# Optimization experiments

Hardware: AMD Instinct MI355X
Metric: run time of the kernel (lower is better)

The kernel has to match this reference:

```python
import jax, jax.numpy as jnp
import numpy as np
from jax import lax

V, Dm, NL, N, K, E = 32000, 1024, 4, 16, 4, 2
Di = Dm * E
B, T = 1, 2048
EPS = 1e-5


def setup_inputs() -> dict:
    key = jax.random.key(0)
    ks = jax.random.split(key, 8)
    s = 0.02
    A_init = jnp.log(jnp.arange(1.0, N + 1, dtype=jnp.float32))  # (N,)
    return {
        "idx": jax.random.randint(ks[0], (B, T), 0, V),
        "emb": jax.random.normal(ks[1], (V, Dm), dtype=jnp.float32) * s,
        "norm_w": jnp.ones((NL, Dm), jnp.float32),
        "in_proj_w": jax.random.normal(ks[2], (NL, 2 * Di, Dm), dtype=jnp.float32) * s,
        "conv_w": jax.random.normal(ks[3], (NL, Di, 1, K), dtype=jnp.float32) * s,
        "conv_b": jnp.zeros((NL, Di), jnp.float32),
        "x_proj_w": jax.random.normal(ks[4], (NL, 2 * N + 1, Di), dtype=jnp.float32) * s,
        "dt_proj_w": jax.random.normal(ks[5], (NL, Di, 1), dtype=jnp.float32) * s,
        "dt_proj_b": jnp.zeros((NL, Di), jnp.float32),
        "A_log": jnp.broadcast_to(A_init[None, None, :], (NL, Di, N)).copy(),
        "D_param": jnp.ones((NL, Di), jnp.float32),
        "out_proj_w": jax.random.normal(ks[6], (NL, Dm, Di), dtype=jnp.float32) * s,
        "norm_f_w": jnp.ones((Dm,), jnp.float32),
    }


def _rmsnorm(x, w):
    rms = jnp.sqrt(jnp.mean(x * x, axis=-1, keepdims=True) + EPS)
    return x / rms * w


def _mamba_block(x, in_w, cw, cb, xp_w, dt_w, dt_b, A_log, Dp, out_w):
    # x: (B, L, Dm)
    xz = x @ in_w.T                       # (B, L, 2*Di)
    x_ssm, z = xz[..., :Di], xz[..., Di:]
    # causal depthwise conv (torch pads both sides then crops -> left-pad only)
    xc = x_ssm.transpose(0, 2, 1)         # (B, Di, L)
    xc = lax.conv_general_dilated(
        xc, cw, window_strides=(1,), padding=[(K - 1, 0)],
        dimension_numbers=("NCH", "OIH", "NCH"), feature_group_count=Di)
    xc = xc + cb[None, :, None]
    u = jax.nn.silu(xc.transpose(0, 2, 1))  # (B, L, Di)
    # selective SSM
    A = -jnp.exp(A_log)                     # (Di, N)
    xp = u @ xp_w.T                         # (B, L, 2N+1)
    dt_raw, Bv, Cv = xp[..., :1], xp[..., 1:1 + N], xp[..., 1 + N:]
    dt = jax.nn.softplus(dt_raw * dt_w[:, 0] + dt_b)  # (B, L, Di)

    def step(h, inp):
        dt_t, Bv_t, Cv_t, u_t = inp          # (B,Di),(B,N),(B,N),(B,Di)
        dA = jnp.exp(dt_t[..., None] * A)    # (B, Di, N)
        h = dA * h + (dt_t * u_t)[..., None] * Bv_t[:, None, :]
        y_t = jnp.einsum("bdn,bn->bd", h, Cv_t)
        return h, y_t

    h0 = jnp.zeros((x.shape[0], Di, N), u.dtype)
    xs = (dt.transpose(1, 0, 2), Bv.transpose(1, 0, 2),
          Cv.transpose(1, 0, 2), u.transpose(1, 0, 2))
    _, ys = lax.scan(step, h0, xs)           # (L, B, Di)
    y = ys.transpose(1, 0, 2) + u * Dp
    y = y * jax.nn.silu(z)
    return y @ out_w.T


def reference(idx, emb, norm_w, in_proj_w, conv_w, conv_b, x_proj_w,
              dt_proj_w, dt_proj_b, A_log, D_param, out_proj_w, norm_f_w):
    x = emb[idx]                             # (B, T, Dm); dropout=0 in eval
    for l in range(NL):
        x = x + _mamba_block(_rmsnorm(x, norm_w[l]), in_proj_w[l], conv_w[l],
                             conv_b[l], x_proj_w[l], dt_proj_w[l], dt_proj_b[l],
                             A_log[l], D_param[l], out_proj_w[l])
    x = _rmsnorm(x, norm_f_w)
    logits = x @ emb.T                       # tied lm_head
    return logits
```

## Files before the change

### kernel.cpp

```cpp
#include <hip/hip_runtime.h>
#include <hip/hip_bf16.h>

typedef __hip_bfloat16 bf16;
typedef __attribute__((ext_vector_type(8))) short short8;
typedef __attribute__((ext_vector_type(4))) float f32x4;

#define TT 2048
#define DM 1024
#define DI 2048
#define NLAYER 4
#define NST 16
#define KC 4
#define VOCAB 32000
#define XPS 33
#define NCHUNK 64
#define CLEN 32

__device__ __forceinline__ float us2f(unsigned short u) {
    union { float f; unsigned int i; } c; c.i = ((unsigned int)u) << 16; return c.f;
}
__device__ __forceinline__ float ldin(const void* p, size_t i, int f32) {
    return f32 ? ((const float*)p)[i] : us2f(((const unsigned short*)p)[i]);
}
__device__ __forceinline__ unsigned short f2us(float f) {
    bf16 h = __float2bfloat16(f);
    return *(unsigned short*)&h;
}

__global__ void detect_kernel(const unsigned int* __restrict__ w_bits, int* __restrict__ flag) {
    if (threadIdx.x == 0) *flag = (w_bits[0] == 0x3F800000u) ? 1 : 0;
}

__global__ void cvt8_kernel(const float* __restrict__ s, unsigned short* __restrict__ d, int n8) {
    int i = blockIdx.x * 256 + threadIdx.x;
    if (i >= n8) return;
    float4 a = ((const float4*)s)[2 * i];
    float4 b = ((const float4*)s)[2 * i + 1];
    unsigned int w0 = (unsigned int)f2us(a.x) | ((unsigned int)f2us(a.y) << 16);
    unsigned int w1 = (unsigned int)f2us(a.z) | ((unsigned int)f2us(a.w) << 16);
    unsigned int w2 = (unsigned int)f2us(b.x) | ((unsigned int)f2us(b.y) << 16);
    unsigned int w3 = (unsigned int)f2us(b.z) | ((unsigned int)f2us(b.w) << 16);
    ((uint4*)d)[i] = make_uint4(w0, w1, w2, w3);
}

__global__ void embed_kernel(const int* __restrict__ idx, const void* __restrict__ emb,
                             float* __restrict__ x, const int* __restrict__ fl) {
    int f32 = *fl;
    int i = blockIdx.x * 256 + threadIdx.x;
    int t = i >> 10, d = i & 1023;
    x[i] = ldin(emb, (size_t)idx[t] * DM + d, f32);
}

__global__ void rmsnorm_kernel(const float* __restrict__ x, const void* __restrict__ w,
                               size_t wofs, bf16* __restrict__ ob, const int* __restrict__ fl) {
    int f32 = *fl;
    int t = blockIdx.x, tid = threadIdx.x;
    float s = 0.f;
    for (int i = tid; i < DM; i += 256) { float v = x[(size_t)t * DM + i]; s += v * v; }
    __shared__ float red[256];
    red[tid] = s; __syncthreads();
    for (int st = 128; st > 0; st >>= 1) { if (tid < st) red[tid] += red[tid + st]; __syncthreads(); }
    float inv = rsqrtf(red[0] / (float)DM + 1e-5f);
    for (int i = tid; i < DM; i += 256) {
        float v = x[(size_t)t * DM + i] * inv * ldin(w, wofs + i, f32);
        ob[(size_t)t * DM + i] = __float2bfloat16(v);
    }
}

__global__ __launch_bounds__(256, 2)
void gemm_mfma(const bf16* __restrict__ A16, const bf16* __restrict__ B16,
               const float* __restrict__ Res, float* __restrict__ Cf, bf16* __restrict__ C16,
               int MT, int NT, int Kk) {
    int Nn = NT << 7;
    __shared__ __align__(16) unsigned short As[128 * 32];
    __shared__ __align__(16) unsigned short Bs[128 * 32];
    int tid = threadIdx.x;
    int w = tid >> 6, lane = tid & 63;
    int h = lane >> 4, r = lane & 15;

    int nwg = MT * NT;
    int bid = blockIdx.x;
    int swz = ((nwg & 7) == 0) ? ((bid & 7) * (nwg >> 3) + (bid >> 3)) : bid;
    int mt = swz % MT, nt = swz / MT;
    int m0 = mt << 7, n0 = nt << 7;

    const unsigned short* Ap = (const unsigned short*)A16;
    const unsigned short* Bp = (const unsigned short*)B16;

    int srow = (w << 5) + (lane >> 2);
    int skof = (lane & 3) << 3;
    const unsigned short* gA = Ap + (size_t)(m0 + srow) * Kk + skof;
    const unsigned short* gB = Bp + (size_t)(n0 + srow) * Kk + skof;
    unsigned short* lA = As + (w << 10);
    unsigned short* lB = Bs + (w << 10);

    f32x4 acc[4][4];
#pragma unroll
    for (int i = 0; i < 4; i++)
#pragma unroll
        for (int j = 0; j < 4; j++) acc[i][j] = (f32x4){0.f, 0.f, 0.f, 0.f};

    int wr = w >> 1, wc = w & 1;
    const unsigned short* rA = As + (((wr << 6) + r) << 5) + (h << 3);
    const unsigned short* rB = Bs + (((wc << 6) + r) << 5) + (h << 3);

    for (int k0 = 0; k0 < Kk; k0 += 32) {
        __builtin_amdgcn_global_load_lds(
            (const __attribute__((address_space(1))) void*)(gA + k0),
            (__attribute__((address_space(3))) void*)lA, 16, 0, 0);
        __builtin_amdgcn_global_load_lds(
            (const __attribute__((address_space(1))) void*)(gA + k0 + (size_t)16 * Kk),
            (__attribute__((address_space(3))) void*)(lA + 512), 16, 0, 0);
        __builtin_amdgcn_global_load_lds(
            (const __attribute__((address_space(1))) void*)(gB + k0),
            (__attribute__((address_space(3))) void*)lB, 16, 0, 0);
        __builtin_amdgcn_global_load_lds(
            (const __attribute__((address_space(1))) void*)(gB + k0 + (size_t)16 * Kk),
            (__attribute__((address_space(3))) void*)(lB + 512), 16, 0, 0);
        __syncthreads();
        short8 af[4], bfr[4];
#pragma unroll
        for (int mi = 0; mi < 4; mi++) af[mi] = *(const short8*)(rA + (mi << 9));
#pragma unroll
        for (int ni = 0; ni < 4; ni++) bfr[ni] = *(const short8*)(rB + (ni << 9));
#pragma unroll
        for (int mi = 0; mi < 4; mi++)
#pragma unroll
            for (int ni = 0; ni < 4; ni++)
                acc[mi][ni] = __builtin_amdgcn_mfma_f32_16x16x32_bf16(
                    af[mi], bfr[ni], acc[mi][ni], 0, 0, 0);
        __syncthreads();
    }
#pragma unroll
    for (int mi = 0; mi < 4; mi++) {
#pragma unroll
        for (int j = 0; j < 4; j++) {
            int row = m0 + (wr << 6) + (mi << 4) + (h << 2) + j;
            size_t base = (size_t)row * Nn + n0 + (wc << 6) + r;
#pragma unroll
            for (int ni = 0; ni < 4; ni++) {
                float v = acc[mi][ni][j];
                size_t o = base + (ni << 4);
                if (Res) v += Res[o];
                if (Cf)  Cf[o] = v;
                if (C16) C16[o] = __float2bfloat16(v);
            }
        }
    }
}

__global__ void convsilu_kernel(const float* __restrict__ xz, const void* __restrict__ cw,
                                size_t cwofs, const void* __restrict__ cb, size_t cbofs,
                                float* __restrict__ u, const int* __restrict__ fl) {
    int f32 = *fl;
    int i = blockIdx.x * 256 + threadIdx.x;
    int t = i >> 11, d = i & 2047;
    float s = ldin(cb, cbofs + d, f32);
#pragma unroll
    for (int j = 0; j < KC; j++) {
        int tt = t - (KC - 1) + j;
        if (tt >= 0) s += ldin(cw, cwofs + d * KC + j, f32) * xz[(size_t)tt * (2 * DI) + d];
    }
    u[i] = s / (1.f + __expf(-s));
}

__global__ void xproj_kernel(const float* __restrict__ u, const void* __restrict__ xpw,
                             size_t wofs, float* __restrict__ xp, const int* __restrict__ fl) {
    int f32 = *fl;
    int t = blockIdx.x, tid = threadIdx.x;
    int w = tid >> 6, lane = tid & 63;
    const float* up = u + (size_t)t * DI + tid * 8;
    float4 u0 = *(const float4*)up;
    float4 u1 = *(const float4*)(up + 4);
    float a0 = u0.x, a1 = u0.y, a2 = u0.z, a3 = u0.w;
    float a4 = u1.x, a5 = u1.y, a6 = u1.z, a7 = u1.w;
    float p[XPS];
    if (f32) {
        const float* wb = (const float*)xpw + wofs + tid * 8;
#pragma unroll
        for (int n = 0; n < XPS; n++) {
            const float* wp = wb + (size_t)n * DI;
            float4 w0 = *(const float4*)wp, w1 = *(const float4*)(wp + 4);
            p[n] = a0 * w0.x + a1 * w0.y + a2 * w0.z + a3 * w0.w
                 + a4 * w1.x + a5 * w1.y + a6 * w1.z + a7 * w1.w;
        }
    } else {
        const unsigned short* wb = (const unsigned short*)xpw + wofs + tid * 8;
#pragma unroll
        for (int n = 0; n < XPS; n++) {
            uint4 wv = *(const uint4*)(wb + (size_t)n * DI);
            p[n] = a0 * us2f(wv.x & 0xffff) + a1 * us2f(wv.x >> 16)
                 + a2 * us2f(wv.y & 0xffff) + a3 * us2f(wv.y >> 16)
                 + a4 * us2f(wv.z & 0xffff) + a5 * us2f(wv.z >> 16)
                 + a6 * us2f(wv.w & 0xffff) + a7 * us2f(wv.w >> 16);
        }
    }
    __shared__ float red[4 * XPS];
#pragma unroll
    for (int n = 0; n < XPS; n++) {
        float v = p[n];
#pragma unroll
        for (int s_ = 1; s_ < 64; s_ <<= 1) v += __shfl_xor(v, s_, 64);
        if (lane == 0) red[w * XPS + n] = v;
    }
    __syncthreads();
    if (tid < XPS)
        xp[t * XPS + tid] = red[tid] + red[XPS + tid] + red[2 * XPS + tid] + red[3 * XPS + tid];
}

__global__ void scanA_kernel(const float* __restrict__ xp, const float* __restrict__ u,
                             const void* __restrict__ dtw, size_t dtwofs,
                             const void* __restrict__ dtb, size_t dtbofs,
                             const void* __restrict__ A_log, size_t aofs,
                             float* __restrict__ S, float* __restrict__ hend,
                             const int* __restrict__ fl) {
    int f32 = *fl;
    int c = blockIdx.y;
    int d = blockIdx.x * 256 + threadIdx.x;
    __shared__ float xps[CLEN * XPS];
    for (int i = threadIdx.x; i < CLEN * XPS; i += 256) xps[i] = xp[c * CLEN * XPS + i];
    __syncthreads();
    float dw = ldin(dtw, dtwofs + d, f32);
    float db = ldin(dtb, dtbofs + d, f32);
    float Ar[NST], hh[NST];
#pragma unroll
    for (int n = 0; n < NST; n++) {
        Ar[n] = -expf(ldin(A_log, aofs + (size_t)d * NST + n, f32));
        hh[n] = 0.f;
    }
    float ssum = 0.f;
    const float* urow = u + (size_t)c * CLEN * DI + d;
    for (int tt = 0; tt < CLEN; tt++) {
        float s = xps[tt * XPS] * dw + db;
        float dtv = (s > 20.f) ? s : log1pf(__expf(s));
        float uv = urow[(size_t)tt * DI];
        float du = dtv * uv;
        ssum += dtv;
        const float* bb = &xps[tt * XPS + 1];
#pragma unroll
        for (int n = 0; n < NST; n++)
            hh[n] = __expf(dtv * Ar[n]) * hh[n] + du * bb[n];
    }
    S[c * DI + d] = ssum;
#pragma unroll
    for (int n = 0; n < NST; n++) hend[((size_t)c * DI + d) * NST + n] = hh[n];
}

__global__ void scanB_kernel(const float* __restrict__ S, float* __restrict__ hend,
                             const void* __restrict__ A_log, size_t aofs,
                             const int* __restrict__ fl) {
    int f32 = *fl;
    int i = blockIdx.x * 256 + threadIdx.x;
    int d = i >> 4;
    float A = -expf(ldin(A_log, aofs + i, f32));
    float H = 0.f;
    for (int c = 0; c < NCHUNK; c++) {
        size_t o = (size_t)c * (DI * NST) + i;
        float he = hend[o];
        hend[o] = H;
        H = __expf(A * S[c * DI + d]) * H + he;
    }
}

__global__ void scanC_kernel(const float* __restrict__ xp, const float* __restrict__ u,
                             const float* __restrict__ xz,
                             const void* __restrict__ dtw, size_t dtwofs,
                             const void* __restrict__ dtb, size_t dtbofs,
                             const void* __restrict__ A_log, size_t aofs,
                             const void* __restrict__ Dp, size_t dofs,
                             const float* __restrict__ hcar, bf16* __restrict__ y16,
                             const int* __restrict__ fl) {
    int f32 = *fl;
    int c = blockIdx.y;
    int d = blockIdx.x * 256 + threadIdx.x;
    __shared__ float xps[CLEN * XPS];
    for (int i = threadIdx.x; i < CLEN * XPS; i += 256) xps[i] = xp[c * CLEN * XPS + i];
    __syncthreads();
    float dw = ldin(dtw, dtwofs + d, f32);
    float db = ldin(dtb, dtbofs + d, f32);
    float Dpv = ldin(Dp, dofs + d, f32);
    float Ar[NST], hh[NST];
#pragma unroll
    for (int n = 0; n < NST; n++) {
        Ar[n] = -expf(ldin(A_log, aofs + (size_t)d * NST + n, f32));
        hh[n] = hcar[((size_t)c * DI + d) * NST + n];
    }
    for (int tt = 0; tt < CLEN; tt++) {
        int t = c * CLEN + tt;
        float s = xps[tt * XPS] * dw + db;
        float dtv = (s > 20.f) ? s : log1pf(__expf(s));
        float uv = u[(size_t)t * DI + d];
        float du = dtv * uv;
        const float* bb = &xps[tt * XPS + 1];
        const float* cc = &xps[tt * XPS + 1 + NST];
        float accv = 0.f;
#pragma unroll
        for (int n = 0; n < NST; n++) {
            hh[n] = __expf(dtv * Ar[n]) * hh[n] + du * bb[n];
            accv += hh[n] * cc[n];
        }
        float z = xz[(size_t)t * (2 * DI) + DI + d];
        float sz = z / (1.f + __expf(-z));
        y16[(size_t)t * DI + d] = __float2bfloat16((accv + uv * Dpv) * sz);
    }
}

extern "C" void kernel_launch(void* const* d_in, const int* in_sizes, int n_in,
                              void* d_out, int out_size, void* d_ws, size_t ws_size,
                              hipStream_t stream) {
    const int*  idx       = (const int*)d_in[0];
    const void* emb       = d_in[1];
    const void* norm_w    = d_in[2];
    const void* in_proj_w = d_in[3];
    const void* conv_w    = d_in[4];
    const void* conv_b    = d_in[5];
    const void* x_proj_w  = d_in[6];
    const void* dt_proj_w = d_in[7];
    const void* dt_proj_b = d_in[8];
    const void* A_log     = d_in[9];
    const void* D_param   = d_in[10];
    const void* out_proj_w= d_in[11];
    const void* norm_f_w  = d_in[12];

    float* ws   = (float*)d_ws;
    float* xz   = ws;
    float* u    = ws + 8388608;
    float* hend = ws + 12582912;
    bf16*  W16A = (bf16*)(ws + 14680064);
    bf16*  W16B = (bf16*)(ws + 16777216);
    float* S    = ws + 17825792;
    float* xp   = ws + 17956864;
    float* x    = ws + 18024448;
    bf16*  xn16 = (bf16*)(ws + 20121600);
    bf16*  y16  = (bf16*)(ws + 21170176);
    int*   fl   = (int*)(ws + 23267328);
    bf16*  emb16= (bf16*)ws;

    long long esz = in_sizes ? (long long)in_sizes[1] : -1;
    int isf32 = (esz == (long long)VOCAB * DM * 2) ? 0 : 1;

    detect_kernel<<<1, 64, 0, stream>>>((const unsigned int*)norm_w, fl);
    embed_kernel<<<TT * DM / 256, 256, 0, stream>>>(idx, emb, x, fl);

    for (int l = 0; l < NLAYER; l++) {
        const bf16* Bin;
        const bf16* Bout;
        if (isf32) {
            cvt8_kernel<<<2 * DI * DM / 8 / 256, 256, 0, stream>>>(
                (const float*)in_proj_w + (size_t)l * 2 * DI * DM,
                (unsigned short*)W16A, 2 * DI * DM / 8);
            cvt8_kernel<<<DM * DI / 8 / 256, 256, 0, stream>>>(
                (const float*)out_proj_w + (size_t)l * DM * DI,
                (unsigned short*)W16B, DM * DI / 8);
            Bin = W16A; Bout = W16B;
        } else {
            Bin  = (const bf16*)in_proj_w  + (size_t)l * 2 * DI * DM;
            Bout = (const bf16*)out_proj_w + (size_t)l * DM * DI;
        }

        rmsnorm_kernel<<<TT, 256, 0, stream>>>(x, norm_w, (size_t)l * DM, xn16, fl);
        gemm_mfma<<<(TT / 128) * (2 * DI / 128), 256, 0, stream>>>(
            xn16, Bin, nullptr, xz, nullptr, TT / 128, 2 * DI / 128, DM);
        convsilu_kernel<<<TT * DI / 256, 256, 0, stream>>>(
            xz, conv_w, (size_t)l * DI * KC, conv_b, (size_t)l * DI, u, fl);
        xproj_kernel<<<TT, 256, 0, stream>>>(u, x_proj_w, (size_t)l * XPS * DI, xp, fl);
        scanA_kernel<<<dim3(DI / 256, NCHUNK), 256, 0, stream>>>(
            xp, u, dt_proj_w, (size_t)l * DI, dt_proj_b, (size_t)l * DI,
            A_log, (size_t)l * DI * NST, S, hend, fl);
        scanB_kernel<<<DI * NST / 256, 256, 0, stream>>>(
            S, hend, A_log, (size_t)l * DI * NST, fl);
        scanC_kernel<<<dim3(DI / 256, NCHUNK), 256, 0, stream>>>(
            xp, u, xz, dt_proj_w, (size_t)l * DI, dt_proj_b, (size_t)l * DI,
            A_log, (size_t)l * DI * NST, D_param, (size_t)l * DI, hend, y16, fl);
        gemm_mfma<<<(TT / 128) * (DM / 128), 256, 0, stream>>>(
            y16, Bout, x, x, nullptr, TT / 128, DM / 128, DI);
    }

    rmsnorm_kernel<<<TT, 256, 0, stream>>>(x, norm_f_w, 0, xn16, fl);

    const bf16* Bemb;
    if (isf32) {
        cvt8_kernel<<<VOCAB * DM / 8 / 256, 256, 0, stream>>>(
            (const float*)emb, (unsigned short*)emb16, VOCAB * DM / 8);
        Bemb = emb16;
    } else {
        Bemb = (const bf16*)emb;
    }
    if (isf32)
        gemm_mfma<<<(TT / 128) * (VOCAB / 128), 256, 0, stream>>>(
            xn16, Bemb, nullptr, (float*)d_out, nullptr, TT / 128, VOCAB / 128, DM);
    else
        gemm_mfma<<<(TT / 128) * (VOCAB / 128), 256, 0, stream>>>(
            xn16, Bemb, nullptr, nullptr, (bf16*)d_out, TT / 128, VOCAB / 128, DM);
}
```

Before: 1.582 ms.

## Fuse conv+xproj, merge weight casts, vectorize norm/embed, template GEMM tile, relayout hend

Fuses the depthwise conv+SiLU with the x_proj reduction into one per-token kernel and merges the two per-layer weight conversion launches into one. Embed and RMSNorm are vectorized with float4 loads, and RMSNorm now reduces with wave shuffles. The GEMM is templated on M tile so out_proj uses 64-row tiles for more workgroups. The chunk-end state buffer is relaid out as [n][chunk][d] so scanB accesses coalesce. Each piece is small, but together they cut launch count and memory traffic; the smaller out_proj tile lowers reuse per block.

```diff
diff --git a/kernel.cpp b/kernel.cpp
--- a/kernel.cpp
+++ b/kernel.cpp
@@ -26,14 +26,20 @@
     bf16 h = __float2bfloat16(f);
     return *(unsigned short*)&h;
 }
+__device__ __forceinline__ size_t hidx(int n, int c, int d) {
+    return ((size_t)n * NCHUNK + c) * DI + d;
+}
 
 __global__ void detect_kernel(const unsigned int* __restrict__ w_bits, int* __restrict__ flag) {
     if (threadIdx.x == 0) *flag = (w_bits[0] == 0x3F800000u) ? 1 : 0;
 }
 
-__global__ void cvt8_kernel(const float* __restrict__ s, unsigned short* __restrict__ d, int n8) {
+__global__ void cvt8_dual_kernel(const float* __restrict__ sA, unsigned short* __restrict__ dA, int n8A,
+                                 const float* __restrict__ sB, unsigned short* __restrict__ dB, int n8B) {
     int i = blockIdx.x * 256 + threadIdx.x;
-    if (i >= n8) return;
+    const float* s; unsigned short* d;
+    if (i < n8A) { s = sA; d = dA; }
+    else { i -= n8A; if (i >= n8B) return; s = sB; d = dB; }
     float4 a = ((const float4*)s)[2 * i];
     float4 b = ((const float4*)s)[2 * i + 1];
     unsigned int w0 = (unsigned int)f2us(a.x) | ((unsigned int)f2us(a.y) << 16);
@@ -46,33 +52,53 @@
 __global__ void embed_kernel(const int* __restrict__ idx, const void* __restrict__ emb,
                              float* __restrict__ x, const int* __restrict__ fl) {
     int f32 = *fl;
-    int i = blockIdx.x * 256 + threadIdx.x;
-    int t = i >> 10, d = i & 1023;
-    x[i] = ldin(emb, (size_t)idx[t] * DM + d, f32);
+    int t = blockIdx.x, q = threadIdx.x;
+    size_t src = (size_t)idx[t] * DM + q * 4;
+    float4 v;
+    if (f32) v = *(const float4*)((const float*)emb + src);
+    else {
+        ushort4 h = *(const ushort4*)((const unsigned short*)emb + src);
+        v = make_float4(us2f(h.x), us2f(h.y), us2f(h.z), us2f(h.w));
+    }
+    ((float4*)x)[(size_t)t * (DM / 4) + q] = v;
 }
 
 __global__ void rmsnorm_kernel(const float* __restrict__ x, const void* __restrict__ w,
                                size_t wofs, bf16* __restrict__ ob, const int* __restrict__ fl) {
     int f32 = *fl;
     int t = blockIdx.x, tid = threadIdx.x;
-    float s = 0.f;
-    for (int i = tid; i < DM; i += 256) { float v = x[(size_t)t * DM + i]; s += v * v; }
-    __shared__ float red[256];
-    red[tid] = s; __syncthreads();
-    for (int st = 128; st > 0; st >>= 1) { if (tid < st) red[tid] += red[tid + st]; __syncthreads(); }
-    float inv = rsqrtf(red[0] / (float)DM + 1e-5f);
-    for (int i = tid; i < DM; i += 256) {
-        float v = x[(size_t)t * DM + i] * inv * ldin(w, wofs + i, f32);
-        ob[(size_t)t * DM + i] = __float2bfloat16(v);
-    }
-}
-
+    int wv = tid >> 6, lane = tid & 63;
+    float4 v = ((const float4*)(x + (size_t)t * DM))[tid];
+    float s = v.x * v.x + v.y * v.y + v.z * v.z + v.w * v.w;
+#pragma unroll
+    for (int o = 1; o < 64; o <<= 1) s += __shfl_xor(s, o, 64);
+    __shared__ float red[4];
+    if (lane == 0) red[wv] = s;
+    __syncthreads();
+    float inv = rsqrtf((red[0] + red[1] + red[2] + red[3]) / (float)DM + 1e-5f);
+    float w0, w1, w2, w3;
+    if (f32) {
+        float4 wq = ((const float4*)((const float*)w + wofs))[tid];
+        w0 = wq.x; w1 = wq.y; w2 = wq.z; w3 = wq.w;
+    } else {
+        ushort4 wq = ((const ushort4*)((const unsigned short*)w + wofs))[tid];
+        w0 = us2f(wq.x); w1 = us2f(wq.y); w2 = us2f(wq.z); w3 = us2f(wq.w);
+    }
+    uint2 o;
+    o.x = (unsigned int)f2us(v.x * inv * w0) | ((unsigned int)f2us(v.y * inv * w1) << 16);
+    o.y = (unsigned int)f2us(v.z * inv * w2) | ((unsigned int)f2us(v.w * inv * w3) << 16);
+    ((uint2*)(ob + (size_t)t * DM))[tid] = o;
+}
+
+template<int BM>
 __global__ __launch_bounds__(256, 2)
 void gemm_mfma(const bf16* __restrict__ A16, const bf16* __restrict__ B16,
                const float* __restrict__ Res, float* __restrict__ Cf, bf16* __restrict__ C16,
                int MT, int NT, int Kk) {
+    constexpr int MR = BM / 32;
+    constexpr int AQ = BM / 64;
     int Nn = NT << 7;
-    __shared__ __align__(16) unsigned short As[128 * 32];
+    __shared__ __align__(16) unsigned short As[BM * 32];
     __shared__ __align__(16) unsigned short Bs[128 * 32];
     int tid = threadIdx.x;
     int w = tid >> 6, lane = tid & 63;
@@ -82,49 +108,48 @@
     int bid = blockIdx.x;
     int swz = ((nwg & 7) == 0) ? ((bid & 7) * (nwg >> 3) + (bid >> 3)) : bid;
     int mt = swz % MT, nt = swz / MT;
-    int m0 = mt << 7, n0 = nt << 7;
+    int m0 = mt * BM, n0 = nt << 7;
 
     const unsigned short* Ap = (const unsigned short*)A16;
     const unsigned short* Bp = (const unsigned short*)B16;
 
-    int srow = (w << 5) + (lane >> 2);
     int skof = (lane & 3) << 3;
-    const unsigned short* gA = Ap + (size_t)(m0 + srow) * Kk + skof;
-    const unsigned short* gB = Bp + (size_t)(n0 + srow) * Kk + skof;
-    unsigned short* lA = As + (w << 10);
+    int srowA = w * (BM / 4) + (lane >> 2);
+    int srowB = (w << 5) + (lane >> 2);
+    const unsigned short* gA = Ap + (size_t)(m0 + srowA) * Kk + skof;
+    const unsigned short* gB = Bp + (size_t)(n0 + srowB) * Kk + skof;
+    unsigned short* lA = As + ((w * (BM / 4)) << 5);
     unsigned short* lB = Bs + (w << 10);
 
-    f32x4 acc[4][4];
-#pragma unroll
-    for (int i = 0; i < 4; i++)
+    f32x4 acc[MR][4];
+#pragma unroll
+    for (int i = 0; i < MR; i++)
 #pragma unroll
         for (int j = 0; j < 4; j++) acc[i][j] = (f32x4){0.f, 0.f, 0.f, 0.f};
 
     int wr = w >> 1, wc = w & 1;
-    const unsigned short* rA = As + (((wr << 6) + r) << 5) + (h << 3);
+    const unsigned short* rA = As + (((wr * (BM / 2)) + r) << 5) + (h << 3);
     const unsigned short* rB = Bs + (((wc << 6) + r) << 5) + (h << 3);
 
     for (int k0 = 0; k0 < Kk; k0 += 32) {
-        __builtin_amdgcn_global_load_lds(
-            (const __attribute__((address_space(1))) void*)(gA + k0),
-            (__attribute__((address_space(3))) void*)lA, 16, 0, 0);
-        __builtin_amdgcn_global_load_lds(
-            (const __attribute__((address_space(1))) void*)(gA + k0 + (size_t)16 * Kk),
-            (__attribute__((address_space(3))) void*)(lA + 512), 16, 0, 0);
-        __builtin_amdgcn_global_load_lds(
-            (const __attribute__((address_space(1))) void*)(gB + k0),
-            (__attribute__((address_space(3))) void*)lB, 16, 0, 0);
-        __builtin_amdgcn_global_load_lds(
-            (const __attribute__((address_space(1))) void*)(gB + k0 + (size_t)16 * Kk),
-            (__attribute__((address_space(3))) void*)(lB + 512), 16, 0, 0);
+#pragma unroll
+        for (int q = 0; q < AQ; q++)
+            __builtin_amdgcn_global_load_lds(
+                (const __attribute__((address_space(1))) void*)(gA + k0 + (size_t)(q * 16) * Kk),
+                (__attribute__((address_space(3))) void*)(lA + q * 512), 16, 0, 0);
+#pragma unroll
+        for (int q = 0; q < 2; q++)
+            __builtin_amdgcn_global_load_lds(
+                (const __attribute__((address_space(1))) void*)(gB + k0 + (size_t)(q * 16) * Kk),
+                (__attribute__((address_space(3))) void*)(lB + q * 512), 16, 0, 0);
         __syncthreads();
-        short8 af[4], bfr[4];
-#pragma unroll
-        for (int mi = 0; mi < 4; mi++) af[mi] = *(const short8*)(rA + (mi << 9));
+        short8 af[MR], bfr[4];
+#pragma unroll
+        for (int mi = 0; mi < MR; mi++) af[mi] = *(const short8*)(rA + (mi << 9));
 #pragma unroll
         for (int ni = 0; ni < 4; ni++) bfr[ni] = *(const short8*)(rB + (ni << 9));
 #pragma unroll
-        for (int mi = 0; mi < 4; mi++)
+        for (int mi = 0; mi < MR; mi++)
 #pragma unroll
             for (int ni = 0; ni < 4; ni++)
                 acc[mi][ni] = __builtin_amdgcn_mfma_f32_16x16x32_bf16(
@@ -132,10 +157,10 @@
         __syncthreads();
     }
 #pragma unroll
-    for (int mi = 0; mi < 4; mi++) {
+    for (int mi = 0; mi < MR; mi++) {
 #pragma unroll
         for (int j = 0; j < 4; j++) {
-            int row = m0 + (wr << 6) + (mi << 4) + (h << 2) + j;
+            int row = m0 + wr * (BM / 2) + (mi << 4) + (h << 2) + j;
             size_t base = (size_t)row * Nn + n0 + (wc << 6) + r;
 #pragma unroll
             for (int ni = 0; ni < 4; ni++) {
@@ -149,50 +174,56 @@
     }
 }
 
-__global__ void convsilu_kernel(const float* __restrict__ xz, const void* __restrict__ cw,
-                                size_t cwofs, const void* __restrict__ cb, size_t cbofs,
-                                float* __restrict__ u, const int* __restrict__ fl) {
-    int f32 = *fl;
-    int i = blockIdx.x * 256 + threadIdx.x;
-    int t = i >> 11, d = i & 2047;
-    float s = ldin(cb, cbofs + d, f32);
+__global__ void cxp_kernel(const float* __restrict__ xz,
+                           const void* __restrict__ cw, size_t cwofs,
+                           const void* __restrict__ cb, size_t cbofs,
+                           const void* __restrict__ xpw, size_t xpwofs,
+                           float* __restrict__ u, float* __restrict__ xp,
+                           const int* __restrict__ fl) {
+    int f32 = *fl;
+    int t = blockIdx.x, tid = threadIdx.x;
+    int wv = tid >> 6, lane = tid & 63;
+    int d0 = tid * 8;
+    float uv[8];
+#pragma unroll
+    for (int k = 0; k < 8; k++) uv[k] = ldin(cb, cbofs + d0 + k, f32);
 #pragma unroll
     for (int j = 0; j < KC; j++) {
         int tt = t - (KC - 1) + j;
-        if (tt >= 0) s += ldin(cw, cwofs + d * KC + j, f32) * xz[(size_t)tt * (2 * DI) + d];
-    }
-    u[i] = s / (1.f + __expf(-s));
-}
-
-__global__ void xproj_kernel(const float* __restrict__ u, const void* __restrict__ xpw,
-                             size_t wofs, float* __restrict__ xp, const int* __restrict__ fl) {
-    int f32 = *fl;
-    int t = blockIdx.x, tid = threadIdx.x;
-    int w = tid >> 6, lane = tid & 63;
-    const float* up = u + (size_t)t * DI + tid * 8;
-    float4 u0 = *(const float4*)up;
-    float4 u1 = *(const float4*)(up + 4);
-    float a0 = u0.x, a1 = u0.y, a2 = u0.z, a3 = u0.w;
-    float a4 = u1.x, a5 = u1.y, a6 = u1.z, a7 = u1.w;
+        if (tt < 0) continue;
+        const float* row = xz + (size_t)tt * (2 * DI) + d0;
+        float4 v0 = *(const float4*)row;
+        float4 v1 = *(const float4*)(row + 4);
+        float vv[8] = {v0.x, v0.y, v0.z, v0.w, v1.x, v1.y, v1.z, v1.w};
+#pragma unroll
+        for (int k = 0; k < 8; k++)
+            uv[k] += ldin(cw, cwofs + (size_t)(d0 + k) * KC + j, f32) * vv[k];
+    }
+#pragma unroll
+    for (int k = 0; k < 8; k++) { float s = uv[k]; uv[k] = s / (1.f + __expf(-s)); }
+    float* ur = u + (size_t)t * DI + d0;
+    *(float4*)ur       = make_float4(uv[0], uv[1], uv[2], uv[3]);
+    *(float4*)(ur + 4) = make_float4(uv[4], uv[5], uv[6], uv[7]);
+
     float p[XPS];
     if (f32) {
-        const float* wb = (const float*)xpw + wofs + tid * 8;
+        const float* wb = (const float*)xpw + xpwofs + d0;
 #pragma unroll
         for (int n = 0; n < XPS; n++) {
             const float* wp = wb + (size_t)n * DI;
             float4 w0 = *(const float4*)wp, w1 = *(const float4*)(wp + 4);
-            p[n] = a0 * w0.x + a1 * w0.y + a2 * w0.z + a3 * w0.w
-                 + a4 * w1.x + a5 * w1.y + a6 * w1.z + a7 * w1.w;
+            p[n] = uv[0] * w0.x + uv[1] * w0.y + uv[2] * w0.z + uv[3] * w0.w
+                 + uv[4] * w1.x + uv[5] * w1.y + uv[6] * w1.z + uv[7] * w1.w;
         }
     } else {
-        const unsigned short* wb = (const unsigned short*)xpw + wofs + tid * 8;
+        const unsigned short* wb = (const unsigned short*)xpw + xpwofs + d0;
 #pragma unroll
         for (int n = 0; n < XPS; n++) {
-            uint4 wv = *(const uint4*)(wb + (size_t)n * DI);
-            p[n] = a0 * us2f(wv.x & 0xffff) + a1 * us2f(wv.x >> 16)
-                 + a2 * us2f(wv.y & 0xffff) + a3 * us2f(wv.y >> 16)
-                 + a4 * us2f(wv.z & 0xffff) + a5 * us2f(wv.z >> 16)
-                 + a6 * us2f(wv.w & 0xffff) + a7 * us2f(wv.w >> 16);
+            uint4 wq = *(const uint4*)(wb + (size_t)n * DI);
+            p[n] = uv[0] * us2f(wq.x & 0xffff) + uv[1] * us2f(wq.x >> 16)
+                 + uv[2] * us2f(wq.y & 0xffff) + uv[3] * us2f(wq.y >> 16)
+                 + uv[4] * us2f(wq.z & 0xffff) + uv[5] * us2f(wq.z >> 16)
+                 + uv[6] * us2f(wq.w & 0xffff) + uv[7] * us2f(wq.w >> 16);
         }
     }
     __shared__ float red[4 * XPS];
@@ -201,7 +232,7 @@
         float v = p[n];
 #pragma unroll
         for (int s_ = 1; s_ < 64; s_ <<= 1) v += __shfl_xor(v, s_, 64);
-        if (lane == 0) red[w * XPS + n] = v;
+        if (lane == 0) red[wv * XPS + n] = v;
     }
     __syncthreads();
     if (tid < XPS)
@@ -233,8 +264,8 @@
     for (int tt = 0; tt < CLEN; tt++) {
         float s = xps[tt * XPS] * dw + db;
         float dtv = (s > 20.f) ? s : log1pf(__expf(s));
-        float uv = urow[(size_t)tt * DI];
-        float du = dtv * uv;
+        float uvv = urow[(size_t)tt * DI];
+        float du = dtv * uvv;
         ssum += dtv;
         const float* bb = &xps[tt * XPS + 1];
 #pragma unroll
@@ -243,7 +274,7 @@
     }
     S[c * DI + d] = ssum;
 #pragma unroll
-    for (int n = 0; n < NST; n++) hend[((size_t)c * DI + d) * NST + n] = hh[n];
+    for (int n = 0; n < NST; n++) hend[hidx(n, c, d)] = hh[n];
 }
 
 __global__ void scanB_kernel(const float* __restrict__ S, float* __restrict__ hend,
@@ -251,11 +282,11 @@
                              const int* __restrict__ fl) {
     int f32 = *fl;
     int i = blockIdx.x * 256 + threadIdx.x;
-    int d = i >> 4;
-    float A = -expf(ldin(A_log, aofs + i, f32));
+    int d = i & (DI - 1), n = i >> 11;
+    float A = -expf(ldin(A_log, aofs + (size_t)d * NST + n, f32));
     float H = 0.f;
     for (int c = 0; c < NCHUNK; c++) {
-        size_t o = (size_t)c * (DI * NST) + i;
+        size_t o = hidx(n, c, d);
         float he = hend[o];
         hend[o] = H;
         H = __expf(A * S[c * DI + d]) * H + he;
@@ -283,14 +314,14 @@
 #pragma unroll
     for (int n = 0; n < NST; n++) {
         Ar[n] = -expf(ldin(A_log, aofs + (size_t)d * NST + n, f32));
-        hh[n] = hcar[((size_t)c * DI + d) * NST + n];
+        hh[n] = hcar[hidx(n, c, d)];
     }
     for (int tt = 0; tt < CLEN; tt++) {
         int t = c * CLEN + tt;
         float s = xps[tt * XPS] * dw + db;
         float dtv = (s > 20.f) ? s : log1pf(__expf(s));
-        float uv = u[(size_t)t * DI + d];
-        float du = dtv * uv;
+        float uvv = u[(size_t)t * DI + d];
+        float du = dtv * uvv;
         const float* bb = &xps[tt * XPS + 1];
         const float* cc = &xps[tt * XPS + 1 + NST];
         float accv = 0.f;
@@ -301,7 +332,7 @@
         }
         float z = xz[(size_t)t * (2 * DI) + DI + d];
         float sz = z / (1.f + __expf(-z));
-        y16[(size_t)t * DI + d] = __float2bfloat16((accv + uv * Dpv) * sz);
+        y16[(size_t)t * DI + d] = __float2bfloat16((accv + uvv * Dpv) * sz);
     }
 }
 
@@ -340,18 +371,16 @@
     int isf32 = (esz == (long long)VOCAB * DM * 2) ? 0 : 1;
 
     detect_kernel<<<1, 64, 0, stream>>>((const unsigned int*)norm_w, fl);
-    embed_kernel<<<TT * DM / 256, 256, 0, stream>>>(idx, emb, x, fl);
+    embed_kernel<<<TT, 256, 0, stream>>>(idx, emb, x, fl);
 
     for (int l = 0; l < NLAYER; l++) {
         const bf16* Bin;
         const bf16* Bout;
         if (isf32) {
-            cvt8_kernel<<<2 * DI * DM / 8 / 256, 256, 0, stream>>>(
-                (const float*)in_proj_w + (size_t)l * 2 * DI * DM,
-                (unsigned short*)W16A, 2 * DI * DM / 8);
-            cvt8_kernel<<<DM * DI / 8 / 256, 256, 0, stream>>>(
-                (const float*)out_proj_w + (size_t)l * DM * DI,
-                (unsigned short*)W16B, DM * DI / 8);
+            int n8A = 2 * DI * DM / 8, n8B = DM * DI / 8;
+            cvt8_dual_kernel<<<(n8A + n8B + 255) / 256, 256, 0, stream>>>(
+                (const float*)in_proj_w + (size_t)l * 2 * DI * DM, (unsigned short*)W16A, n8A,
+                (const float*)out_proj_w + (size_t)l * DM * DI, (unsigned short*)W16B, n8B);
             Bin = W16A; Bout = W16B;
         } else {
             Bin  = (const bf16*)in_proj_w  + (size_t)l * 2 * DI * DM;
@@ -359,11 +388,11 @@
         }
 
         rmsnorm_kernel<<<TT, 256, 0, stream>>>(x, norm_w, (size_t)l * DM, xn16, fl);
-        gemm_mfma<<<(TT / 128) * (2 * DI / 128), 256, 0, stream>>>(
+        gemm_mfma<128><<<(TT / 128) * (2 * DI / 128), 256, 0, stream>>>(
             xn16, Bin, nullptr, xz, nullptr, TT / 128, 2 * DI / 128, DM);
-        convsilu_kernel<<<TT * DI / 256, 256, 0, stream>>>(
-            xz, conv_w, (size_t)l * DI * KC, conv_b, (size_t)l * DI, u, fl);
-        xproj_kernel<<<TT, 256, 0, stream>>>(u, x_proj_w, (size_t)l * XPS * DI, xp, fl);
+        cxp_kernel<<<TT, 256, 0, stream>>>(
+            xz, conv_w, (size_t)l * DI * KC, conv_b, (size_t)l * DI,
+            x_proj_w, (size_t)l * XPS * DI, u, xp, fl);
         scanA_kernel<<<dim3(DI / 256, NCHUNK), 256, 0, stream>>>(
             xp, u, dt_proj_w, (size_t)l * DI, dt_proj_b, (size_t)l * DI,
             A_log, (size_t)l * DI * NST, S, hend, fl);
@@ -372,24 +401,25 @@
         scanC_kernel<<<dim3(DI / 256, NCHUNK), 256, 0, stream>>>(
             xp, u, xz, dt_proj_w, (size_t)l * DI, dt_proj_b, (size_t)l * DI,
             A_log, (size_t)l * DI * NST, D_param, (size_t)l * DI, hend, y16, fl);
-        gemm_mfma<<<(TT / 128) * (DM / 128), 256, 0, stream>>>(
-            y16, Bout, x, x, nullptr, TT / 128, DM / 128, DI);
+        gemm_mfma<64><<<(TT / 64) * (DM / 128), 256, 0, stream>>>(
+            y16, Bout, x, x, nullptr, TT / 64, DM / 128, DI);
     }
 
     rmsnorm_kernel<<<TT, 256, 0, stream>>>(x, norm_f_w, 0, xn16, fl);
 
     const bf16* Bemb;
     if (isf32) {
-        cvt8_kernel<<<VOCAB * DM / 8 / 256, 256, 0, stream>>>(
-            (const float*)emb, (unsigned short*)emb16, VOCAB * DM / 8);
+        int n8 = VOCAB * DM / 8;
+        cvt8_dual_kernel<<<(n8 + 255) / 256, 256, 0, stream>>>(
+            (const float*)emb, (unsigned short*)emb16, n8, nullptr, nullptr, 0);
         Bemb = emb16;
     } else {
         Bemb = (const bf16*)emb;
     }
     if (isf32)
-        gemm_mfma<<<(TT / 128) * (VOCAB / 128), 256, 0, stream>>>(
+        gemm_mfma<128><<<(TT / 128) * (VOCAB / 128), 256, 0, stream>>>(
             xn16, Bemb, nullptr, (float*)d_out, nullptr, TT / 128, VOCAB / 128, DM);
     else
-        gemm_mfma<<<(TT / 128) * (VOCAB / 128), 256, 0, stream>>>(
+        gemm_mfma<128><<<(TT / 128) * (VOCAB / 128), 256, 0, stream>>>(
             xn16, Bemb, nullptr, nullptr, (bf16*)d_out, TT / 128, VOCAB / 128, DM);
 }
```

After: 1.554 ms. About the same (-1.8%).
